# Kernel tuning notes

Hardware: AMD Instinct MI355X
Metric: run time of the kernel (lower is better)

## Reference

```python
import jax, jax.numpy as jnp
import numpy as np

N_CLASSES = 40
EMBED_DIM = 128
MOMENTUM = 0.1
LAMBDA_R, LAMBDA_C, LAMBDA_M = 1.0, 0.5, 1.0
BATCH = 262144


def setup_inputs() -> dict:
    key = jax.random.key(0)
    k1, k2, k3 = jax.random.split(key, 3)
    z = jax.random.normal(k1, (BATCH, EMBED_DIM), dtype=jnp.float32)
    y = jax.random.randint(k2, (BATCH,), 0, N_CLASSES)
    centers = jax.random.normal(k3, (N_CLASSES, EMBED_DIM), dtype=jnp.float32)
    initialized = jnp.ones((N_CLASSES,), dtype=bool)
    # buffers derived from class_counts (imbalanced ramp), r0=gamma=m0=1, alpha=0.25
    counts = jnp.asarray([1000.0 * (i + 1) for i in range(N_CLASSES)], jnp.float32)
    n_max = jnp.max(counts)
    target_radii = 1.0 + 1.0 * jnp.log(n_max / (counts + 1.0))
    margins = 1.0 * jnp.power(n_max / (counts + 1.0), 0.25)
    return {"z": z, "y": y, "centers": centers, "initialized": initialized,
            "target_radii": target_radii, "margins": margins}


def _update_centers(z, y, centers, initialized):
    # EMA centroid update on detached embeddings (torch.no_grad equivalent).
    zs = jax.lax.stop_gradient(z)
    sums = jax.ops.segment_sum(zs, y, num_segments=N_CLASSES)            # [C, D]
    cnt = jax.ops.segment_sum(jnp.ones((zs.shape[0],), zs.dtype), y,
                              num_segments=N_CLASSES)                    # [C]
    mean = sums / jnp.maximum(cnt, 1.0)[:, None]
    ema = (1.0 - MOMENTUM) * centers + MOMENTUM * mean
    new = jnp.where(initialized[:, None], ema, mean)                     # first-touch init
    return jnp.where((cnt > 0)[:, None], new, centers)                   # skip empty classes


def reference(z, y, centers, initialized, target_radii, margins):
    c = _update_centers(z, y, centers, initialized)                      # [C, D]

    # radial loss: smooth L1 (beta=1) between ||z|| and per-class target radius
    r = jnp.linalg.norm(z, axis=-1)                                      # [B]
    d = r - target_radii[y]
    ad = jnp.abs(d)
    loss_radial = jnp.mean(jnp.where(ad < 1.0, 0.5 * d * d, ad - 0.5))

    # compact loss: mean squared distance to own centroid
    diff = z - c[y]                                                      # [B, D]
    loss_compact = jnp.mean(jnp.sum(diff * diff, axis=-1))

    # margin loss: min distance to any other class centroid via Gram trick
    z2 = jnp.sum(z * z, axis=-1)                                         # [B]
    c2 = jnp.sum(c * c, axis=-1)                                         # [C]
    d2 = z2[:, None] + c2[None, :] - 2.0 * (z @ c.T)                     # [B, C]
    dist = jnp.sqrt(jnp.maximum(d2, 0.0))
    own = y[:, None] == jnp.arange(N_CLASSES)[None, :]                   # [B, C] bool
    dist_opp = jnp.min(jnp.where(own, jnp.inf, dist), axis=1)            # [B]
    loss_margin = jnp.mean(jax.nn.relu(margins[y] - dist_opp))

    return LAMBDA_R * loss_radial + LAMBDA_C * loss_compact + LAMBDA_M * loss_margin
```

## Files before the change

### kernel.cpp

```cpp
#include <hip/hip_runtime.h>
#include <math.h>

#define BATCH 262144
#define DIM   128
#define NCLS  40
#define NCP   48
#define CD    (NCLS * DIM)

#define TB1 512
#define NB1 256
#define TB3 256
#define NB3 (BATCH / 256)

typedef __attribute__((ext_vector_type(8))) short short8;
typedef __attribute__((ext_vector_type(4))) float f32x4;

__device__ __forceinline__ short f2bf(float f) {
    unsigned u = __float_as_uint(f);
    u += 0x7fffu + ((u >> 16) & 1u);
    return (short)(u >> 16);
}

#define K1_ALL(M) M(0) M(1) M(2) M(3) M(4) M(5) M(6) M(7) M(8) M(9) \
                  M(10) M(11) M(12) M(13) M(14) M(15) M(16) M(17) M(18) M(19) \
                  M(20) M(21) M(22) M(23) M(24) M(25) M(26) M(27) M(28) M(29) \
                  M(30) M(31) M(32) M(33) M(34) M(35) M(36) M(37) M(38) M(39)
#define K1_DECL(c) float2 a##c = {0.0f, 0.0f};
#define K1_CASE(c) case c: a##c.x += vv.x; a##c.y += vv.y; \
    asm volatile("" : "+v"(a##c.x), "+v"(a##c.y)); break;
#define K1_ACCUM(CLS, V) { const float2 vv = (V); \
    switch (CLS) { K1_ALL(K1_CASE) default: break; } }
#define K1_STA(c)  s_bufA[(c) * 64 + lane] = a##c;
#define K1_STB(c)  s_bufB[(c) * 64 + lane] = a##c;
#define K1_RMWA(c) { float2 t_ = s_bufA[(c) * 64 + lane]; \
                     t_.x += a##c.x; t_.y += a##c.y; \
                     s_bufA[(c) * 64 + lane] = t_; }
#define K1_RMWB(c) { float2 t_ = s_bufB[(c) * 64 + lane]; \
                     t_.x += a##c.x; t_.y += a##c.y; \
                     s_bufB[(c) * 64 + lane] = t_; }

__device__ __forceinline__ void k1_stage(const float* src, float* dst) {
    __builtin_amdgcn_global_load_lds(
        (const __attribute__((address_space(1))) void*)src,
        (__attribute__((address_space(3))) void*)dst, 16, 0, 0);
}

__global__ __launch_bounds__(TB1) void k1_segsum(const float* __restrict__ z,
                                                 const int* __restrict__ y,
                                                 float* __restrict__ ps,
                                                 float* __restrict__ gcnt) {
    __shared__ float  s_ring[8][8 * 256];
    __shared__ float2 s_bufA[NCLS * 64];
    __shared__ float2 s_bufB[NCLS * 64];
    __shared__ float  s_cnt[NCLS];

    const int t    = threadIdx.x;
    const int w    = t >> 6;
    const int lane = t & 63;
    if (t < NCLS) s_cnt[t] = 0.0f;
    __syncthreads();

    const int rbase = blockIdx.x * 1024 + w * 128;

    const int2 y2 = *(const int2*)(y + rbase + lane * 2);
    atomicAdd(&s_cnt[y2.x], 1.0f);
    atomicAdd(&s_cnt[y2.y], 1.0f);

    const float* __restrict__ zw = z + (size_t)rbase * DIM;
    float* __restrict__ ringw = s_ring[w];

#pragma unroll
    for (int p = 0; p < 8; ++p)
        k1_stage(zw + (size_t)p * 256 + lane * 4, ringw + p * 256);

    K1_ALL(K1_DECL)

#pragma unroll 1
    for (int p = 0; p < 56; ++p) {
        asm volatile("s_waitcnt vmcnt(7)" ::: "memory");
        __builtin_amdgcn_sched_barrier(0);
        const int slot = p & 7;
        const float2 v0 = *(const float2*)(ringw + slot * 256 + lane * 2);
        const float2 v1 = *(const float2*)(ringw + slot * 256 + 128 + lane * 2);
        const int c0 = __builtin_amdgcn_readlane(y2.x, p);
        const int c1 = __builtin_amdgcn_readlane(y2.y, p);
        K1_ACCUM(c0, v0)
        K1_ACCUM(c1, v1)
        k1_stage(zw + (size_t)(p + 8) * 256 + lane * 4, ringw + slot * 256);
    }

#define K1_TAIL(P, W) { \
        asm volatile("s_waitcnt vmcnt(" #W ")" ::: "memory"); \
        __builtin_amdgcn_sched_barrier(0); \
        const int slot = (P) & 7; \
        const float2 v0 = *(const float2*)(ringw + slot * 256 + lane * 2); \
        const float2 v1 = *(const float2*)(ringw + slot * 256 + 128 + lane * 2); \
        const int c0 = __builtin_amdgcn_readlane(y2.x, (P)); \
        const int c1 = __builtin_amdgcn_readlane(y2.y, (P)); \
        K1_ACCUM(c0, v0) \
        K1_ACCUM(c1, v1) }
    K1_TAIL(56, 7) K1_TAIL(57, 6) K1_TAIL(58, 5) K1_TAIL(59, 4)
    K1_TAIL(60, 3) K1_TAIL(61, 2) K1_TAIL(62, 1) K1_TAIL(63, 0)
#undef K1_TAIL

    __syncthreads();
    if (w == 0) { K1_ALL(K1_STA) }
    if (w == 1) { K1_ALL(K1_STB) }
    __syncthreads();
    if (w == 2) { K1_ALL(K1_RMWA) }
    if (w == 3) { K1_ALL(K1_RMWB) }
    __syncthreads();
    if (w == 4) { K1_ALL(K1_RMWA) }
    if (w == 5) { K1_ALL(K1_RMWB) }
    __syncthreads();
    if (w == 6) { K1_ALL(K1_RMWA) }
    if (w == 7) { K1_ALL(K1_RMWB) }
    __syncthreads();

    float2* __restrict__ psb = (float2*)(ps + (size_t)blockIdx.x * CD);
    for (int i = t; i < NCLS * 64; i += TB1) {
        const float2 A = s_bufA[i], B = s_bufB[i];
        psb[i] = make_float2(A.x + B.x, A.y + B.y);
    }
    if (t < NCLS) atomicAdd(&gcnt[t], s_cnt[t]);
}

__global__ __launch_bounds__(512) void k2_centers(const float* __restrict__ ps,
                                                  const float* __restrict__ gcnt,
                                                  const float* __restrict__ centers,
                                                  short* __restrict__ cbf,
                                                  float* __restrict__ c2p) {
    const int j    = blockIdx.x >> 1;
    const int half = blockIdx.x & 1;
    const int t    = threadIdx.x;
    const int dl   = t & 63;
    const int d    = half * 64 + dl;
    const int s    = t >> 6;

    if (j >= NCLS) {
        if (s == 0) cbf[j * DIM + d] = 0;
        if (t == 0) c2p[blockIdx.x] = 5e29f;
        return;
    }

    const float* __restrict__ p = ps + j * DIM + d + (size_t)(s * 32) * CD;
    float sum = 0.0f;
#pragma unroll 8
    for (int b = 0; b < 32; ++b) sum += p[(size_t)b * CD];

    __shared__ float red[512];
    red[t] = sum;
    __syncthreads();

    if (s == 0) {
        float tot = 0.0f;
#pragma unroll
        for (int k = 0; k < 8; ++k) tot += red[(k << 6) | dl];
        const float cnt  = gcnt[j];
        const float mean = tot / fmaxf(cnt, 1.0f);
        const float ctr  = centers[j * DIM + d];
        const float ema  = 0.9f * ctr + 0.1f * mean;
        const float cv   = (cnt > 0.0f) ? ema : ctr;
        cbf[j * DIM + d] = f2bf(cv);
        red[t] = cv * cv;
    }
    __syncthreads();
    if (t == 0) {
        float sc = 0.0f;
#pragma unroll 8
        for (int i = 0; i < 64; ++i) sc += red[i];
        c2p[blockIdx.x] = sc;
    }
}

__global__ __launch_bounds__(TB3) void k3_loss(const float* __restrict__ z,
                                               const int* __restrict__ y,
                                               const short* __restrict__ cbf,
                                               const float* __restrict__ c2p,
                                               const float* __restrict__ tr,
                                               const float* __restrict__ mg,
                                               float* __restrict__ out) {
    __shared__ float s_S[4][64 * 52];
    __shared__ float s_c2[NCP];

    const int t = threadIdx.x;
    if (t < NCP) s_c2[t] = c2p[2 * t] + c2p[2 * t + 1];

    const int w    = t >> 6;
    const int lane = t & 63;
    const int q    = lane >> 4;
    const int col  = lane & 15;
    const int wavebase = blockIdx.x * 256 + w * 64;

    short8 bfrag[3][4];
#pragma unroll
    for (int ct = 0; ct < 3; ++ct)
#pragma unroll
        for (int s = 0; s < 4; ++s)
            bfrag[ct][s] = *(const short8*)(cbf + (ct * 16 + col) * DIM + s * 32 + q * 8);

    __syncthreads();

#pragma unroll 1
    for (int rt = 0; rt < 4; ++rt) {
        const float* __restrict__ zrow =
            z + (size_t)(wavebase + rt * 16 + col) * DIM + q * 8;

        float4 f[8];
#pragma unroll
        for (int s = 0; s < 4; ++s) {
            f[2 * s]     = *(const float4*)(zrow + s * 32);
            f[2 * s + 1] = *(const float4*)(zrow + s * 32 + 4);
        }

        float zp = 0.0f;
#pragma unroll
        for (int i = 0; i < 8; ++i) {
            zp = fmaf(f[i].x, f[i].x, zp);
            zp = fmaf(f[i].y, f[i].y, zp);
            zp = fmaf(f[i].z, f[i].z, zp);
            zp = fmaf(f[i].w, f[i].w, zp);
        }

        short8 afr[4];
#pragma unroll
        for (int s = 0; s < 4; ++s) {
            const float4 f0 = f[2 * s], f1 = f[2 * s + 1];
            afr[s][0] = f2bf(f0.x); afr[s][1] = f2bf(f0.y);
            afr[s][2] = f2bf(f0.z); afr[s][3] = f2bf(f0.w);
            afr[s][4] = f2bf(f1.x); afr[s][5] = f2bf(f1.y);
            afr[s][6] = f2bf(f1.z); afr[s][7] = f2bf(f1.w);
        }

        f32x4 acc0 = {0.f, 0.f, 0.f, 0.f};
        f32x4 acc1 = {0.f, 0.f, 0.f, 0.f};
        f32x4 acc2 = {0.f, 0.f, 0.f, 0.f};
#pragma unroll
        for (int s = 0; s < 4; ++s) {
            acc0 = __builtin_amdgcn_mfma_f32_16x16x32_bf16(afr[s], bfrag[0][s], acc0, 0, 0, 0);
            acc1 = __builtin_amdgcn_mfma_f32_16x16x32_bf16(afr[s], bfrag[1][s], acc1, 0, 0, 0);
            acc2 = __builtin_amdgcn_mfma_f32_16x16x32_bf16(afr[s], bfrag[2][s], acc2, 0, 0, 0);
        }

        zp += __shfl_xor(zp, 16);
        zp += __shfl_xor(zp, 32);
        if (q == 0) s_S[w][(rt * 16 + col) * 52 + 48] = zp;

#pragma unroll
        for (int reg = 0; reg < 4; ++reg) {
            const int rr = rt * 16 + q * 4 + reg;
            s_S[w][rr * 52 + col]      = acc0[reg];
            s_S[w][rr * 52 + 16 + col] = acc1[reg];
            s_S[w][rr * 52 + 32 + col] = acc2[reg];
        }
    }

    const int row = blockIdx.x * 256 + t;
    const int cls = y[row];
    const float z2v = s_S[w][lane * 52 + 48];

    float own_d2 = 0.0f;
    float mind2  = 3.4e38f;
#pragma unroll
    for (int k = 0; k < 12; ++k) {
        const float4 Sv = *(const float4*)&s_S[w][lane * 52 + 4 * k];
        const float Se[4] = {Sv.x, Sv.y, Sv.z, Sv.w};
#pragma unroll
        for (int e = 0; e < 4; ++e) {
            const int j = 4 * k + e;
            float d2 = fmaxf(z2v + s_c2[j] - 2.0f * Se[e], 0.0f);
            const bool isown = (j == cls);
            own_d2 = isown ? d2 : own_d2;
            mind2  = isown ? mind2 : fminf(mind2, d2);
        }
    }

    const float r  = sqrtf(z2v);
    const float dd = r - tr[cls];
    const float ad = fabsf(dd);
    const float rad = (ad < 1.0f) ? 0.5f * dd * dd : ad - 0.5f;

    const float dist = sqrtf(mind2);
    const float marg = fmaxf(mg[cls] - dist, 0.0f);

    const float tot = rad + 0.5f * own_d2 + marg;

    __syncthreads();
    float* s_red = &s_S[0][0];
    s_red[t] = tot;
    __syncthreads();
    for (int off = TB3 / 2; off > 0; off >>= 1) {
        if (t < off) s_red[t] += s_red[t + off];
        __syncthreads();
    }
    if (t == 0) atomicAdd(out, s_red[0] * (1.0f / (float)BATCH));
}

extern "C" void kernel_launch(void* const* d_in, const int* in_sizes, int n_in,
                              void* d_out, int out_size, void* d_ws, size_t ws_size,
                              hipStream_t stream) {
    const float* z       = (const float*)d_in[0];
    const int*   y       = (const int*)d_in[1];
    const float* centers = (const float*)d_in[2];
    const float* tr      = (const float*)d_in[4];
    const float* mg      = (const float*)d_in[5];
    float* out = (float*)d_out;

    float* ws        = (float*)d_ws;
    float* part_sums = ws;
    float* c2p       = part_sums + (size_t)NB1 * CD;
    float* gcnt      = c2p + 2 * NCP;
    short* cbf       = (short*)(gcnt + NCLS);

    hipMemsetAsync(gcnt, 0, NCLS * sizeof(float), stream);
    hipMemsetAsync(out, 0, sizeof(float), stream);

    k1_segsum<<<NB1, TB1, 0, stream>>>(z, y, part_sums, gcnt);
    k2_centers<<<2 * NCP, 512, 0, stream>>>(part_sums, gcnt, centers, cbf, c2p);
    k3_loss<<<NB3, TB3, 0, stream>>>(z, y, cbf, c2p, tr, mg, out);
}
```

Baseline: 274.7 us.

## Rewrite segment-sum kernel with per-wave LDS accumulators and register prefetch

The k1 segment-sum kernel drops the 40-way register switch with global_load_lds ring buffering. Each of 4 waves now keeps a full class×dim accumulator in LDS and does read-modify-write per row, with float4 register prefetch 8 rows ahead. When both rows in a pair share a class they are combined by cross-half shuffle first. This removes switch divergence and the multi-stage LDS reduction, but adds serialized LDS RMW traffic, 80KB LDS per block which limits occupancy, and a smaller block size.

Result: faster. 240.2 us (-12.5%).

```diff
diff --git a/kernel.cpp b/kernel.cpp
--- a/kernel.cpp
+++ b/kernel.cpp
@@ -7,7 +7,7 @@
 #define NCP   48
 #define CD    (NCLS * DIM)
 
-#define TB1 512
+#define TB1 256
 #define NB1 256
 #define TB3 256
 #define NB3 (BATCH / 256)
@@ -21,106 +21,96 @@
     return (short)(u >> 16);
 }
 
-#define K1_ALL(M) M(0) M(1) M(2) M(3) M(4) M(5) M(6) M(7) M(8) M(9) \
-                  M(10) M(11) M(12) M(13) M(14) M(15) M(16) M(17) M(18) M(19) \
-                  M(20) M(21) M(22) M(23) M(24) M(25) M(26) M(27) M(28) M(29) \
-                  M(30) M(31) M(32) M(33) M(34) M(35) M(36) M(37) M(38) M(39)
-#define K1_DECL(c) float2 a##c = {0.0f, 0.0f};
-#define K1_CASE(c) case c: a##c.x += vv.x; a##c.y += vv.y; \
-    asm volatile("" : "+v"(a##c.x), "+v"(a##c.y)); break;
-#define K1_ACCUM(CLS, V) { const float2 vv = (V); \
-    switch (CLS) { K1_ALL(K1_CASE) default: break; } }
-#define K1_STA(c)  s_bufA[(c) * 64 + lane] = a##c;
-#define K1_STB(c)  s_bufB[(c) * 64 + lane] = a##c;
-#define K1_RMWA(c) { float2 t_ = s_bufA[(c) * 64 + lane]; \
-                     t_.x += a##c.x; t_.y += a##c.y; \
-                     s_bufA[(c) * 64 + lane] = t_; }
-#define K1_RMWB(c) { float2 t_ = s_bufB[(c) * 64 + lane]; \
-                     t_.x += a##c.x; t_.y += a##c.y; \
-                     s_bufB[(c) * 64 + lane] = t_; }
-
-__device__ __forceinline__ void k1_stage(const float* src, float* dst) {
-    __builtin_amdgcn_global_load_lds(
-        (const __attribute__((address_space(1))) void*)src,
-        (__attribute__((address_space(3))) void*)dst, 16, 0, 0);
-}
-
 __global__ __launch_bounds__(TB1) void k1_segsum(const float* __restrict__ z,
                                                  const int* __restrict__ y,
                                                  float* __restrict__ ps,
                                                  float* __restrict__ gcnt) {
-    __shared__ float  s_ring[8][8 * 256];
-    __shared__ float2 s_bufA[NCLS * 64];
-    __shared__ float2 s_bufB[NCLS * 64];
-    __shared__ float  s_cnt[NCLS];
+    __shared__ float s_acc[4][NCLS * DIM];
+    __shared__ float s_cnt[NCLS];
 
     const int t    = threadIdx.x;
     const int w    = t >> 6;
     const int lane = t & 63;
-    if (t < NCLS) s_cnt[t] = 0.0f;
-    __syncthreads();
-
-    const int rbase = blockIdx.x * 1024 + w * 128;
-
-    const int2 y2 = *(const int2*)(y + rbase + lane * 2);
-    atomicAdd(&s_cnt[y2.x], 1.0f);
-    atomicAdd(&s_cnt[y2.y], 1.0f);
+
+    {
+        float4* az = (float4*)&s_acc[0][0];
+        const float4 z4 = make_float4(0.f, 0.f, 0.f, 0.f);
+        for (int i = t; i < 4 * NCLS * DIM / 4; i += TB1) az[i] = z4;
+        if (t < NCLS) s_cnt[t] = 0.0f;
+    }
+    __syncthreads();
+
+    const int rbase = blockIdx.x * 1024 + w * 256;
+
+    const int2 yA = ((const int2*)(y + rbase))[lane];
+    const int2 yB = ((const int2*)(y + rbase + 128))[lane];
+    atomicAdd(&s_cnt[yA.x], 1.0f);
+    atomicAdd(&s_cnt[yA.y], 1.0f);
+    atomicAdd(&s_cnt[yB.x], 1.0f);
+    atomicAdd(&s_cnt[yB.y], 1.0f);
 
     const float* __restrict__ zw = z + (size_t)rbase * DIM;
-    float* __restrict__ ringw = s_ring[w];
-
-#pragma unroll
-    for (int p = 0; p < 8; ++p)
-        k1_stage(zw + (size_t)p * 256 + lane * 4, ringw + p * 256);
-
-    K1_ALL(K1_DECL)
-
-#pragma unroll 1
-    for (int p = 0; p < 56; ++p) {
-        asm volatile("s_waitcnt vmcnt(7)" ::: "memory");
-        __builtin_amdgcn_sched_barrier(0);
-        const int slot = p & 7;
-        const float2 v0 = *(const float2*)(ringw + slot * 256 + lane * 2);
-        const float2 v1 = *(const float2*)(ringw + slot * 256 + 128 + lane * 2);
-        const int c0 = __builtin_amdgcn_readlane(y2.x, p);
-        const int c1 = __builtin_amdgcn_readlane(y2.y, p);
-        K1_ACCUM(c0, v0)
-        K1_ACCUM(c1, v1)
-        k1_stage(zw + (size_t)(p + 8) * 256 + lane * 4, ringw + slot * 256);
-    }
-
-#define K1_TAIL(P, W) { \
-        asm volatile("s_waitcnt vmcnt(" #W ")" ::: "memory"); \
-        __builtin_amdgcn_sched_barrier(0); \
-        const int slot = (P) & 7; \
-        const float2 v0 = *(const float2*)(ringw + slot * 256 + lane * 2); \
-        const float2 v1 = *(const float2*)(ringw + slot * 256 + 128 + lane * 2); \
-        const int c0 = __builtin_amdgcn_readlane(y2.x, (P)); \
-        const int c1 = __builtin_amdgcn_readlane(y2.y, (P)); \
-        K1_ACCUM(c0, v0) \
-        K1_ACCUM(c1, v1) }
-    K1_TAIL(56, 7) K1_TAIL(57, 6) K1_TAIL(58, 5) K1_TAIL(59, 4)
-    K1_TAIL(60, 3) K1_TAIL(61, 2) K1_TAIL(62, 1) K1_TAIL(63, 0)
-#undef K1_TAIL
-
-    __syncthreads();
-    if (w == 0) { K1_ALL(K1_STA) }
-    if (w == 1) { K1_ALL(K1_STB) }
-    __syncthreads();
-    if (w == 2) { K1_ALL(K1_RMWA) }
-    if (w == 3) { K1_ALL(K1_RMWB) }
-    __syncthreads();
-    if (w == 4) { K1_ALL(K1_RMWA) }
-    if (w == 5) { K1_ALL(K1_RMWB) }
-    __syncthreads();
-    if (w == 6) { K1_ALL(K1_RMWA) }
-    if (w == 7) { K1_ALL(K1_RMWB) }
-    __syncthreads();
-
-    float2* __restrict__ psb = (float2*)(ps + (size_t)blockIdx.x * CD);
-    for (int i = t; i < NCLS * 64; i += TB1) {
-        const float2 A = s_bufA[i], B = s_bufB[i];
-        psb[i] = make_float2(A.x + B.x, A.y + B.y);
+    float* __restrict__ accw = s_acc[w];
+
+    float4 vb[8];
+#pragma unroll
+    for (int q = 0; q < 8; ++q)
+        vb[q] = *(const float4*)(zw + (size_t)q * 256 + lane * 4);
+
+#define K1_HALF(YH, GB, CLAMP)                                                \
+    _Pragma("unroll 1")                                                       \
+    for (int i0 = 0; i0 < 64; i0 += 8) {                                      \
+        _Pragma("unroll")                                                     \
+        for (int q = 0; q < 8; ++q) {                                         \
+            const int i2 = i0 + q;                                            \
+            float4 v = vb[q];                                                 \
+            int g = (GB) + i2 + 8;                                            \
+            if (CLAMP && g > 127) g = (GB) + i2;    \
+            vb[q] = *(const float4*)(zw + (size_t)g * 256 + lane * 4);        \
+            const int c0 = __builtin_amdgcn_readlane((YH).x, i2);             \
+            const int c1 = __builtin_amdgcn_readlane((YH).y, i2);             \
+            if (c0 != c1) {       \
+                const int cls = (lane < 32) ? c0 : c1;                        \
+                float4* ap = (float4*)&accw[cls * DIM] + (lane & 31);         \
+                float4 o = *ap;                                               \
+                o.x += v.x; o.y += v.y; o.z += v.z; o.w += v.w;               \
+                *ap = o;                                                      \
+            } else {           \
+                v.x += __shfl_xor(v.x, 32);                                   \
+                v.y += __shfl_xor(v.y, 32);                                   \
+                v.z += __shfl_xor(v.z, 32);                                   \
+                v.w += __shfl_xor(v.w, 32);                                   \
+                if (lane < 32) {                                              \
+                    float4* ap = (float4*)&accw[c0 * DIM] + lane;             \
+                    float4 o = *ap;                                           \
+                    o.x += v.x; o.y += v.y; o.z += v.z; o.w += v.w;           \
+                    *ap = o;                                                  \
+                }                                                             \
+            }                                                                 \
+        }                                                                     \
+    }
+
+    K1_HALF(yA, 0, 0)
+    K1_HALF(yB, 64, 1)
+#undef K1_HALF
+
+    __syncthreads();
+
+    float4* __restrict__ psb = (float4*)(ps + (size_t)blockIdx.x * CD);
+    const float4* a0 = (const float4*)s_acc[0];
+    const float4* a1 = (const float4*)s_acc[1];
+    const float4* a2 = (const float4*)s_acc[2];
+    const float4* a3 = (const float4*)s_acc[3];
+#pragma unroll
+    for (int k = 0; k < 5; ++k) {
+        const int j = t + k * TB1;
+        const float4 p0 = a0[j], p1 = a1[j], p2 = a2[j], p3 = a3[j];
+        float4 r;
+        r.x = (p0.x + p1.x) + (p2.x + p3.x);
+        r.y = (p0.y + p1.y) + (p2.y + p3.y);
+        r.z = (p0.z + p1.z) + (p2.z + p3.z);
+        r.w = (p0.w + p1.w) + (p2.w + p3.w);
+        psb[j] = r;
     }
     if (t < NCLS) atomicAdd(&gcnt[t], s_cnt[t]);
 }
```
